# Kernel tuning notes

Hardware: AMD Instinct MI355X
Metric: run time of the kernel (lower is better)

The kernel has to match this reference:

```python
import jax, jax.numpy as jnp
import numpy as np

C = 512
NUM_HEADS = 8


def setup_inputs() -> dict:
    key = jax.random.key(0)
    ks = jax.random.split(key, 9)
    s = 1.0 / np.sqrt(C)
    inp = {
        "x": jax.random.normal(ks[0], (2, C, 64, 64), dtype=jnp.float32),
        "Wq": jax.random.uniform(ks[1], (C, C), jnp.float32, -s, s),
        "bq": jax.random.uniform(ks[2], (C,), jnp.float32, -s, s),
        "Wk": jax.random.uniform(ks[3], (C, C), jnp.float32, -s, s),
        "bk": jax.random.uniform(ks[4], (C,), jnp.float32, -s, s),
        "Wv": jax.random.uniform(ks[5], (C, C), jnp.float32, -s, s),
        "bv": jax.random.uniform(ks[6], (C,), jnp.float32, -s, s),
        "Wp": jax.random.uniform(ks[7], (C, C), jnp.float32, -s, s),
        "bp": jax.random.uniform(ks[8], (C,), jnp.float32, -s, s),
    }
    return inp


def _split_heads(t):
    # [B, S, C] -> [B, h, S, d]
    B, S, Ct = t.shape
    return t.reshape(B, S, NUM_HEADS, Ct // NUM_HEADS).transpose(0, 2, 1, 3)


def reference(x, Wq, bq, Wk, bk, Wv, bv, Wp, bp):
    B, Ct, H, W = x.shape
    tok = x.transpose(0, 2, 3, 1).reshape(B, H * W, Ct)  # [B, S, C]
    q = _split_heads(tok @ Wq.T + bq)
    k = _split_heads(tok @ Wk.T + bk)
    v = _split_heads(tok @ Wv.T + bv)
    d = q.shape[-1]
    scores = jnp.einsum("bhsd,bhtd->bhst", q, k) / jnp.sqrt(jnp.float32(d))
    attn = jax.nn.softmax(scores, axis=-1)
    out = jnp.einsum("bhst,bhtd->bhsd", attn, v)
    out = out.transpose(0, 2, 1, 3).reshape(B, H * W, Ct)  # merge heads
    out = out @ Wp.T + bp
    return out.reshape(B, H, W, Ct).transpose(0, 3, 1, 2)
```

## Files before the change

kernel.cpp:

```cpp
#include <hip/hip_runtime.h>
#include <stdint.h>
#include <math.h>

typedef unsigned short u16;
typedef uint32_t u32;
typedef short bf16x8 __attribute__((ext_vector_type(8)));
typedef float f32x4  __attribute__((ext_vector_type(4)));

#define DEV __device__ __forceinline__

DEV u16 f2bf(float f) {
    union { float f; u32 u; } x; x.f = f;
    u32 lsb = (x.u >> 16) & 1u;
    x.u += 0x7fffu + lsb;
    return (u16)(x.u >> 16);
}

DEV u32 pack2(float a, float b) {
    union { float f; u32 u; } x, y; x.f = a; y.f = b;
    return __builtin_amdgcn_perm(y.u + 0x8000u, x.u + 0x8000u, 0x07060302u);
}

#if __has_builtin(__builtin_amdgcn_exp2f)
DEV float fexp2(float x) { return __builtin_amdgcn_exp2f(x); }
#else
DEV float fexp2(float x) { return __expf(x * 0.69314718056f); }
#endif

DEV f32x4 mfma16(bf16x8 a, bf16x8 b, f32x4 c) {
    return __builtin_amdgcn_mfma_f32_16x16x32_bf16(a, b, c, 0, 0, 0);
}

__global__ __launch_bounds__(256) void prep_kernel(const float* __restrict__ x,
                                                   u16* __restrict__ tok,
                                                   const float* __restrict__ w0,
                                                   const float* __restrict__ w1,
                                                   const float* __restrict__ w2,
                                                   const float* __restrict__ w3,
                                                   u16* __restrict__ dst) {
    __shared__ u16 t[64][65];
    const int id = blockIdx.x, tid = threadIdx.x;
    if (id < 1024) {
        const int b = id >> 9, c0 = ((id >> 6) & 7) * 64, s0 = (id & 63) * 64;
        const float* xb = x + ((size_t)b * 512 + c0) * 4096 + s0;
        u16* tb = tok + ((size_t)b * 4096 + s0) * 512 + c0;
        {
            const int jc = tid & 15, i0 = tid >> 4;
#pragma unroll
            for (int ii = 0; ii < 4; ii++) {
                int i = i0 * 4 + ii;
                float4 v = *(const float4*)&xb[(size_t)i * 4096 + jc * 4];
                t[i][jc * 4 + 0] = f2bf(v.x);
                t[i][jc * 4 + 1] = f2bf(v.y);
                t[i][jc * 4 + 2] = f2bf(v.z);
                t[i][jc * 4 + 3] = f2bf(v.w);
            }
        }
        __syncthreads();
        {
            const int j = tid & 31, i0 = tid >> 5;
#pragma unroll
            for (int ii = 0; ii < 8; ii++) {
                int srow = i0 * 8 + ii;
                u32 v = (u32)t[j * 2][srow] | ((u32)t[j * 2 + 1][srow] << 16);
                *(u32*)(&tb[(size_t)srow * 512 + j * 2]) = v;
            }
        }
    } else {
        const int id2 = id - 1024;
        const int j = id2 >> 8;
        const float* src = (j == 0) ? w0 : (j == 1) ? w1 : (j == 2) ? w2 : w3;
        int idx = ((id2 & 255) * 256 + tid) * 4;
        float4 v = *(const float4*)&src[idx];
        uint2 pv;
        pv.x = pack2(v.x, v.y);
        pv.y = pack2(v.z, v.w);
        *(uint2*)&dst[(size_t)j * 262144 + idx] = pv;
    }
}

DEV void proj_core(const u16* __restrict__ W, const float* __restrict__ bias,
                   const u16* __restrict__ Bb, void* __restrict__ out,
                   int b, int mode, float scale,
                   u16 (*__restrict__ Alds)[4096], u16 (*__restrict__ Blds)[4096]) {
    const int tid = threadIdx.x;
    const int wave = tid >> 6, lane = tid & 63, q = lane >> 4, c = lane & 15;
    const int m0 = blockIdx.y * 128, n0 = blockIdx.x * 128;

    const int cs = tid & 15, qs = (tid >> 4) & 3, ms = (tid >> 6) & 3;
    const u16* Asrc0 = W  + (size_t)(m0 + ms * 16 + cs) * 512 + qs * 8;
    const u16* Asrc1 = W  + (size_t)(m0 + (ms + 4) * 16 + cs) * 512 + qs * 8;
    const u16* Bsrc0 = Bb + (size_t)(n0 + ms * 16 + cs) * 512 + qs * 8;
    const u16* Bsrc1 = Bb + (size_t)(n0 + (ms + 4) * 16 + cs) * 512 + qs * 8;

    f32x4 acc[4][4] = {};

    int4 pa0 = *(const int4*)&Asrc0[0];
    int4 pa1 = *(const int4*)&Asrc1[0];
    int4 pb0 = *(const int4*)&Bsrc0[0];
    int4 pb1 = *(const int4*)&Bsrc1[0];
    int4 ha0 = *(const int4*)&Asrc0[32];
    int4 ha1 = *(const int4*)&Asrc1[32];
    int4 hb0 = *(const int4*)&Bsrc0[32];
    int4 hb1 = *(const int4*)&Bsrc1[32];
    *(int4*)&Alds[0][tid * 8]         = pa0;
    *(int4*)&Alds[0][(tid + 256) * 8] = pa1;
    *(int4*)&Blds[0][tid * 8]         = pb0;
    *(int4*)&Blds[0][(tid + 256) * 8] = pb1;
    __syncthreads();

    int p = 0, pw = 1;
    for (int it = 0; it < 16; it++) {
        const int kn = ((it + 2) & 15) * 32;

        int4 na0 = *(const int4*)&Asrc0[kn];
        int4 na1 = *(const int4*)&Asrc1[kn];
        int4 nb0 = *(const int4*)&Bsrc0[kn];
        int4 nb1 = *(const int4*)&Bsrc1[kn];

        bf16x8 af[4], bfr[4];
#pragma unroll
        for (int t = 0; t < 4; t++) {
            int gm = (((wave & 1) * 4 + t) * 4 + q) * 16 + c;
            af[t] = *(const bf16x8*)&Alds[p][gm * 8];
            int gn = (((wave >> 1) * 4 + t) * 4 + q) * 16 + c;
            bfr[t] = *(const bf16x8*)&Blds[p][gn * 8];
        }
#pragma unroll
        for (int mt = 0; mt < 4; mt++)
#pragma unroll
            for (int nt = 0; nt < 4; nt++)
                acc[mt][nt] = mfma16(af[mt], bfr[nt], acc[mt][nt]);

        *(int4*)&Alds[pw][tid * 8]         = ha0;
        *(int4*)&Alds[pw][(tid + 256) * 8] = ha1;
        *(int4*)&Blds[pw][tid * 8]         = hb0;
        *(int4*)&Blds[pw][(tid + 256) * 8] = hb1;
        ha0 = na0; ha1 = na1; hb0 = nb0; hb1 = nb1;
        __syncthreads();
        p = pw; pw = (pw == 2) ? 0 : pw + 1;
    }

    const int mbase = m0 + (wave & 1) * 64, nbase = n0 + (wave >> 1) * 64;
#pragma unroll
    for (int mt = 0; mt < 4; mt++) {
        int co0 = mbase + mt * 16 + q * 4;
        float b0 = bias[co0 + 0], b1 = bias[co0 + 1];
        float b2 = bias[co0 + 2], b3 = bias[co0 + 3];
#pragma unroll
        for (int nt = 0; nt < 4; nt++) {
            int scol = nbase + nt * 16 + c;
            float v0 = (acc[mt][nt][0] + b0) * scale;
            float v1 = (acc[mt][nt][1] + b1) * scale;
            float v2 = (acc[mt][nt][2] + b2) * scale;
            float v3 = (acc[mt][nt][3] + b3) * scale;
            if (mode == 0) {
                uint2 pv; pv.x = pack2(v0, v1); pv.y = pack2(v2, v3);
                size_t idx = ((size_t)(b * 8 + (co0 >> 6)) * 4096 + scol) * 64 + (co0 & 63);
                *(uint2*)&((u16*)out)[idx] = pv;
            } else if (mode == 1) {
                u16* o = (u16*)out;
                o[((size_t)(b * 512 + co0 + 0)) * 4096 + scol] = f2bf(v0);
                o[((size_t)(b * 512 + co0 + 1)) * 4096 + scol] = f2bf(v1);
                o[((size_t)(b * 512 + co0 + 2)) * 4096 + scol] = f2bf(v2);
                o[((size_t)(b * 512 + co0 + 3)) * 4096 + scol] = f2bf(v3);
            } else {
                float* o = (float*)out;
                o[((size_t)(b * 512 + co0 + 0)) * 4096 + scol] = v0;
                o[((size_t)(b * 512 + co0 + 1)) * 4096 + scol] = v1;
                o[((size_t)(b * 512 + co0 + 2)) * 4096 + scol] = v2;
                o[((size_t)(b * 512 + co0 + 3)) * 4096 + scol] = v3;
            }
        }
    }
}

__global__ __launch_bounds__(256) void qkv_kernel(const u16* __restrict__ Wbf,
                                                  const float* __restrict__ bq,
                                                  const float* __restrict__ bk,
                                                  const float* __restrict__ bv,
                                                  const u16* __restrict__ tok,
                                                  u16* __restrict__ Qb,
                                                  u16* __restrict__ Kb,
                                                  u16* __restrict__ Vb) {
    __shared__ u16 Alds[3][4096];
    __shared__ u16 Blds[3][4096];
    const int z = blockIdx.z, j = z >> 1, b = z & 1;
    const u16* W = Wbf + (size_t)j * 262144;
    const float* bias = (j == 0) ? bq : (j == 1) ? bk : bv;
    void* out = (j == 0) ? (void*)Qb : (j == 1) ? (void*)Kb : (void*)Vb;
    const float scale = (j == 0) ? 0.1803368801f : 1.0f;
    const int mode = (j == 2) ? 1 : 0;
    proj_core(W, bias, tok + (size_t)b * (4096 * 512), out, b, mode, scale, Alds, Blds);
}

__global__ __launch_bounds__(256) void projp_kernel(const u16* __restrict__ Wp,
                                                    const float* __restrict__ bp,
                                                    const u16* __restrict__ attout,
                                                    float* __restrict__ out) {
    __shared__ u16 Alds[3][4096];
    __shared__ u16 Blds[3][4096];
    const int b = blockIdx.z;
    proj_core(Wp, bp, attout + (size_t)b * (4096 * 512), out, b, 2, 1.0f, Alds, Blds);
}

__global__ __launch_bounds__(256) void attn_kernel(const u16* __restrict__ Qm,
                                                   const u16* __restrict__ Km,
                                                   const u16* __restrict__ Vm,
                                                   u16* __restrict__ attout) {
    __shared__ u16 Klds[2][4096];
    __shared__ u16 Vlds[2][4096];
    __shared__ u16 Plds[128 * 72];
    const int tid = threadIdx.x, wave = tid >> 6, lane = tid & 63;
    const int q = lane >> 4, c = lane & 15;
    const int bhd = blockIdx.y, s0 = blockIdx.x * 128;
    const u16* Qb = Qm + (size_t)bhd * (4096 * 64);
    const u16* Kb = Km + (size_t)bhd * (4096 * 64);
    const u16* Vb = Vm + (size_t)bhd * (64 * 4096);

    bf16x8 qf[2][2];
#pragma unroll
    for (int st = 0; st < 2; st++)
#pragma unroll
        for (int kd = 0; kd < 2; kd++)
            qf[st][kd] = *(const bf16x8*)
                &Qb[(size_t)(s0 + wave * 32 + st * 16 + c) * 64 + kd * 32 + q * 8];

    const int rr = tid & 15, qq = (tid >> 4) & 3, kk = (tid >> 6) & 1;
    const int t40 = tid >> 7, t41 = t40 + 2;
    const u16* Ksrc0 = Kb + (size_t)(t40 * 16 + rr) * 64 + kk * 32 + qq * 8;
    const u16* Ksrc1 = Kb + (size_t)(t41 * 16 + rr) * 64 + kk * 32 + qq * 8;
    const u16* Vsrc0 = Vb + (size_t)(t40 * 16 + rr) * 4096 + kk * 32 + qq * 8;
    const u16* Vsrc1 = Vb + (size_t)(t41 * 16 + rr) * 4096 + kk * 32 + qq * 8;
    u16* Prow = &Plds[(size_t)(wave * 32 + c) * 72];

    f32x4 oacc[4][2] = {};
    float lsum[2] = {0.f, 0.f};

    *(int4*)&Klds[0][tid * 8]         = *(const int4*)&Ksrc0[0];
    *(int4*)&Klds[0][(tid + 256) * 8] = *(const int4*)&Ksrc1[0];
    *(int4*)&Vlds[0][tid * 8]         = *(const int4*)&Vsrc0[0];
    *(int4*)&Vlds[0][(tid + 256) * 8] = *(const int4*)&Vsrc1[0];
    __syncthreads();

    for (int it = 0; it < 64; it++) {
        const int p = it & 1;
        const size_t t0n = (size_t)(((it + 1) & 63) * 64);

        int4 kst0 = *(const int4*)&Ksrc0[t0n * 64];
        int4 kst1 = *(const int4*)&Ksrc1[t0n * 64];
        int4 vst0 = *(const int4*)&Vsrc0[t0n];
        int4 vst1 = *(const int4*)&Vsrc1[t0n];

        f32x4 sacc[4][2] = {};
#pragma unroll
        for (int kd = 0; kd < 2; kd++) {
            bf16x8 ka[4];
#pragma unroll
            for (int tt = 0; tt < 4; tt++)
                ka[tt] = *(const bf16x8*)&Klds[p][(((tt * 2 + kd) * 4 + q) * 16 + c) * 8];
#pragma unroll
            for (int tt = 0; tt < 4; tt++)
#pragma unroll
                for (int st = 0; st < 2; st++)
                    sacc[tt][st] = mfma16(ka[tt], qf[st][kd], sacc[tt][st]);
        }

#pragma unroll
        for (int st = 0; st < 2; st++) {
#pragma unroll
            for (int tt = 0; tt < 4; tt++) {
                float p0 = fexp2(sacc[tt][st][0]);
                float p1 = fexp2(sacc[tt][st][1]);
                float p2 = fexp2(sacc[tt][st][2]);
                float p3 = fexp2(sacc[tt][st][3]);
                lsum[st] += (p0 + p1) + (p2 + p3);
                uint2 pv; pv.x = pack2(p0, p1); pv.y = pack2(p2, p3);
                *(uint2*)&Prow[st * (16 * 72) + tt * 16 + q * 4] = pv;
            }
        }

#pragma unroll
        for (int kt = 0; kt < 2; kt++) {
            bf16x8 va[4], pb[2];
#pragma unroll
            for (int dt = 0; dt < 4; dt++)
                va[dt] = *(const bf16x8*)&Vlds[p][(((dt * 2 + kt) * 4 + q) * 16 + c) * 8];
#pragma unroll
            for (int st = 0; st < 2; st++)
                pb[st] = *(const bf16x8*)&Prow[st * (16 * 72) + kt * 32 + q * 8];
#pragma unroll
            for (int dt = 0; dt < 4; dt++)
#pragma unroll
                for (int st = 0; st < 2; st++)
                    oacc[dt][st] = mfma16(va[dt], pb[st], oacc[dt][st]);
        }

        *(int4*)&Klds[1 - p][tid * 8]         = kst0;
        *(int4*)&Klds[1 - p][(tid + 256) * 8] = kst1;
        *(int4*)&Vlds[1 - p][tid * 8]         = vst0;
        *(int4*)&Vlds[1 - p][(tid + 256) * 8] = vst1;
        __syncthreads();
    }

    const int b = bhd >> 3, hd = bhd & 7;
#pragma unroll
    for (int st = 0; st < 2; st++) {
        float l = lsum[st];
        l += __shfl_xor(l, 16, 64);
        l += __shfl_xor(l, 32, 64);
        float rl = 1.0f / l;
        int s = s0 + wave * 32 + st * 16 + c;
#pragma unroll
        for (int dt = 0; dt < 4; dt++) {
            uint2 pv;
            pv.x = pack2(oacc[dt][st][0] * rl, oacc[dt][st][1] * rl);
            pv.y = pack2(oacc[dt][st][2] * rl, oacc[dt][st][3] * rl);
            size_t idx = ((size_t)(b * 4096 + s)) * 512 + hd * 64 + dt * 16 + q * 4;
            *(uint2*)&attout[idx] = pv;
        }
    }
}

extern "C" void kernel_launch(void* const* d_in, const int* in_sizes, int n_in,
                              void* d_out, int out_size, void* d_ws, size_t ws_size,
                              hipStream_t stream) {
    (void)in_sizes; (void)n_in; (void)out_size; (void)ws_size;
    const float* x  = (const float*)d_in[0];
    const float* Wq = (const float*)d_in[1];
    const float* bq = (const float*)d_in[2];
    const float* Wk = (const float*)d_in[3];
    const float* bk = (const float*)d_in[4];
    const float* Wv = (const float*)d_in[5];
    const float* bv = (const float*)d_in[6];
    const float* Wp = (const float*)d_in[7];
    const float* bp = (const float*)d_in[8];
    float* out = (float*)d_out;

    const size_t NTOK = (size_t)4 * 1024 * 1024;
    u16* tok = (u16*)d_ws;
    u16* Qb  = tok + NTOK;
    u16* Kb  = Qb + NTOK;
    u16* Vb  = Kb + NTOK;
    u16* Wbf = Vb + NTOK;
    u16* attout = tok;

    prep_kernel<<<dim3(2048), 256, 0, stream>>>(x, tok, Wq, Wk, Wv, Wp, Wbf);
    qkv_kernel<<<dim3(32, 4, 6), 256, 0, stream>>>(Wbf, bq, bk, bv, tok, Qb, Kb, Vb);
    attn_kernel<<<dim3(32, 16), 256, 0, stream>>>(Qb, Kb, Vb, attout);
    projp_kernel<<<dim3(32, 4, 2), 256, 0, stream>>>(Wbf + 3 * 262144, bp, attout, out);
}
```

Measured before the change: 224.4 us.

## Fuse all stages into one persistent cooperative kernel with grid syncs

Replaces the four separate launches (prep, QKV projection, attention, output projection) with a single 512-block cooperative kernel. Grid-wide syncs separate the phases, and a static job assignment gives 256 blocks a second QKV tile. The stages share one LDS buffer, and a fallback launches the same kernel four times with a phase argument if the cooperative launch fails. The goal is to remove inter-kernel launch gaps and tail drain. The risks are grid-sync overhead, uneven work in the QKV phase, and register and occupancy limits set by the heaviest phase.

```diff
diff --git a/kernel.cpp b/kernel.cpp
--- a/kernel.cpp
+++ b/kernel.cpp
@@ -1,6 +1,9 @@
 #include <hip/hip_runtime.h>
+#include <hip/hip_cooperative_groups.h>
 #include <stdint.h>
 #include <math.h>
+
+namespace cg = cooperative_groups;
 
 typedef unsigned short u16;
 typedef uint32_t u32;
@@ -31,61 +34,55 @@
     return __builtin_amdgcn_mfma_f32_16x16x32_bf16(a, b, c, 0, 0, 0);
 }
 
-__global__ __launch_bounds__(256) void prep_kernel(const float* __restrict__ x,
-                                                   u16* __restrict__ tok,
-                                                   const float* __restrict__ w0,
-                                                   const float* __restrict__ w1,
-                                                   const float* __restrict__ w2,
-                                                   const float* __restrict__ w3,
-                                                   u16* __restrict__ dst) {
-    __shared__ u16 t[64][65];
-    const int id = blockIdx.x, tid = threadIdx.x;
-    if (id < 1024) {
-        const int b = id >> 9, c0 = ((id >> 6) & 7) * 64, s0 = (id & 63) * 64;
-        const float* xb = x + ((size_t)b * 512 + c0) * 4096 + s0;
-        u16* tb = tok + ((size_t)b * 4096 + s0) * 512 + c0;
-        {
-            const int jc = tid & 15, i0 = tid >> 4;
-#pragma unroll
-            for (int ii = 0; ii < 4; ii++) {
-                int i = i0 * 4 + ii;
-                float4 v = *(const float4*)&xb[(size_t)i * 4096 + jc * 4];
-                t[i][jc * 4 + 0] = f2bf(v.x);
-                t[i][jc * 4 + 1] = f2bf(v.y);
-                t[i][jc * 4 + 2] = f2bf(v.z);
-                t[i][jc * 4 + 3] = f2bf(v.w);
-            }
-        }
-        __syncthreads();
-        {
-            const int j = tid & 31, i0 = tid >> 5;
-#pragma unroll
-            for (int ii = 0; ii < 8; ii++) {
-                int srow = i0 * 8 + ii;
-                u32 v = (u32)t[j * 2][srow] | ((u32)t[j * 2 + 1][srow] << 16);
-                *(u32*)(&tb[(size_t)srow * 512 + j * 2]) = v;
-            }
-        }
-    } else {
-        const int id2 = id - 1024;
-        const int j = id2 >> 8;
-        const float* src = (j == 0) ? w0 : (j == 1) ? w1 : (j == 2) ? w2 : w3;
-        int idx = ((id2 & 255) * 256 + tid) * 4;
-        float4 v = *(const float4*)&src[idx];
-        uint2 pv;
-        pv.x = pack2(v.x, v.y);
-        pv.y = pack2(v.z, v.w);
-        *(uint2*)&dst[(size_t)j * 262144 + idx] = pv;
-    }
-}
-
-DEV void proj_core(const u16* __restrict__ W, const float* __restrict__ bias,
+DEV void do_transpose(int id, const float* __restrict__ x, u16* __restrict__ tok,
+                      u16* __restrict__ t) {
+    const int tid = threadIdx.x;
+    const int b = id >> 9, c0 = ((id >> 6) & 7) * 64, s0 = (id & 63) * 64;
+    const float* xb = x + ((size_t)b * 512 + c0) * 4096 + s0;
+    u16* tb = tok + ((size_t)b * 4096 + s0) * 512 + c0;
+    {
+        const int jc = tid & 15, i0 = tid >> 4;
+#pragma unroll
+        for (int ii = 0; ii < 4; ii++) {
+            int i = i0 * 4 + ii;
+            float4 v = *(const float4*)&xb[(size_t)i * 4096 + jc * 4];
+            t[i * 65 + jc * 4 + 0] = f2bf(v.x);
+            t[i * 65 + jc * 4 + 1] = f2bf(v.y);
+            t[i * 65 + jc * 4 + 2] = f2bf(v.z);
+            t[i * 65 + jc * 4 + 3] = f2bf(v.w);
+        }
+    }
+    __syncthreads();
+    {
+        const int j = tid & 31, i0 = tid >> 5;
+#pragma unroll
+        for (int ii = 0; ii < 8; ii++) {
+            int srow = i0 * 8 + ii;
+            u32 v = (u32)t[(j * 2) * 65 + srow] | ((u32)t[(j * 2 + 1) * 65 + srow] << 16);
+            *(u32*)(&tb[(size_t)srow * 512 + j * 2]) = v;
+        }
+    }
+}
+
+DEV void do_wconv(int id, const float* __restrict__ w0, const float* __restrict__ w1,
+                  const float* __restrict__ w2, const float* __restrict__ w3,
+                  u16* __restrict__ dst) {
+    const int j = id >> 8;
+    const float* src = (j == 0) ? w0 : (j == 1) ? w1 : (j == 2) ? w2 : w3;
+    int idx = ((id & 255) * 256 + threadIdx.x) * 4;
+    float4 v = *(const float4*)&src[idx];
+    uint2 pv;
+    pv.x = pack2(v.x, v.y);
+    pv.y = pack2(v.z, v.w);
+    *(uint2*)&dst[(size_t)j * 262144 + idx] = pv;
+}
+
+DEV void proj_tile(const u16* __restrict__ W, const float* __restrict__ bias,
                    const u16* __restrict__ Bb, void* __restrict__ out,
-                   int b, int mode, float scale,
-                   u16 (*__restrict__ Alds)[4096], u16 (*__restrict__ Blds)[4096]) {
+                   int b, int mode, float scale, int m0, int n0,
+                   u16* __restrict__ Ab, u16* __restrict__ Bl) {
     const int tid = threadIdx.x;
     const int wave = tid >> 6, lane = tid & 63, q = lane >> 4, c = lane & 15;
-    const int m0 = blockIdx.y * 128, n0 = blockIdx.x * 128;
 
     const int cs = tid & 15, qs = (tid >> 4) & 3, ms = (tid >> 6) & 3;
     const u16* Asrc0 = W  + (size_t)(m0 + ms * 16 + cs) * 512 + qs * 8;
@@ -103,10 +100,10 @@
     int4 ha1 = *(const int4*)&Asrc1[32];
     int4 hb0 = *(const int4*)&Bsrc0[32];
     int4 hb1 = *(const int4*)&Bsrc1[32];
-    *(int4*)&Alds[0][tid * 8]         = pa0;
-    *(int4*)&Alds[0][(tid + 256) * 8] = pa1;
-    *(int4*)&Blds[0][tid * 8]         = pb0;
-    *(int4*)&Blds[0][(tid + 256) * 8] = pb1;
+    *(int4*)&Ab[tid * 8]         = pa0;
+    *(int4*)&Ab[(tid + 256) * 8] = pa1;
+    *(int4*)&Bl[tid * 8]         = pb0;
+    *(int4*)&Bl[(tid + 256) * 8] = pb1;
     __syncthreads();
 
     int p = 0, pw = 1;
@@ -122,9 +119,9 @@
 #pragma unroll
         for (int t = 0; t < 4; t++) {
             int gm = (((wave & 1) * 4 + t) * 4 + q) * 16 + c;
-            af[t] = *(const bf16x8*)&Alds[p][gm * 8];
+            af[t] = *(const bf16x8*)&Ab[p * 4096 + gm * 8];
             int gn = (((wave >> 1) * 4 + t) * 4 + q) * 16 + c;
-            bfr[t] = *(const bf16x8*)&Blds[p][gn * 8];
+            bfr[t] = *(const bf16x8*)&Bl[p * 4096 + gn * 8];
         }
 #pragma unroll
         for (int mt = 0; mt < 4; mt++)
@@ -132,10 +129,10 @@
             for (int nt = 0; nt < 4; nt++)
                 acc[mt][nt] = mfma16(af[mt], bfr[nt], acc[mt][nt]);
 
-        *(int4*)&Alds[pw][tid * 8]         = ha0;
-        *(int4*)&Alds[pw][(tid + 256) * 8] = ha1;
-        *(int4*)&Blds[pw][tid * 8]         = hb0;
-        *(int4*)&Blds[pw][(tid + 256) * 8] = hb1;
+        *(int4*)&Ab[pw * 4096 + tid * 8]         = ha0;
+        *(int4*)&Ab[pw * 4096 + (tid + 256) * 8] = ha1;
+        *(int4*)&Bl[pw * 4096 + tid * 8]         = hb0;
+        *(int4*)&Bl[pw * 4096 + (tid + 256) * 8] = hb1;
         ha0 = na0; ha1 = na1; hb0 = nb0; hb1 = nb1;
         __syncthreads();
         p = pw; pw = (pw == 2) ? 0 : pw + 1;
@@ -175,45 +172,12 @@
     }
 }
 
-__global__ __launch_bounds__(256) void qkv_kernel(const u16* __restrict__ Wbf,
-                                                  const float* __restrict__ bq,
-                                                  const float* __restrict__ bk,
-                                                  const float* __restrict__ bv,
-                                                  const u16* __restrict__ tok,
-                                                  u16* __restrict__ Qb,
-                                                  u16* __restrict__ Kb,
-                                                  u16* __restrict__ Vb) {
-    __shared__ u16 Alds[3][4096];
-    __shared__ u16 Blds[3][4096];
-    const int z = blockIdx.z, j = z >> 1, b = z & 1;
-    const u16* W = Wbf + (size_t)j * 262144;
-    const float* bias = (j == 0) ? bq : (j == 1) ? bk : bv;
-    void* out = (j == 0) ? (void*)Qb : (j == 1) ? (void*)Kb : (void*)Vb;
-    const float scale = (j == 0) ? 0.1803368801f : 1.0f;
-    const int mode = (j == 2) ? 1 : 0;
-    proj_core(W, bias, tok + (size_t)b * (4096 * 512), out, b, mode, scale, Alds, Blds);
-}
-
-__global__ __launch_bounds__(256) void projp_kernel(const u16* __restrict__ Wp,
-                                                    const float* __restrict__ bp,
-                                                    const u16* __restrict__ attout,
-                                                    float* __restrict__ out) {
-    __shared__ u16 Alds[3][4096];
-    __shared__ u16 Blds[3][4096];
-    const int b = blockIdx.z;
-    proj_core(Wp, bp, attout + (size_t)b * (4096 * 512), out, b, 2, 1.0f, Alds, Blds);
-}
-
-__global__ __launch_bounds__(256) void attn_kernel(const u16* __restrict__ Qm,
-                                                   const u16* __restrict__ Km,
-                                                   const u16* __restrict__ Vm,
-                                                   u16* __restrict__ attout) {
-    __shared__ u16 Klds[2][4096];
-    __shared__ u16 Vlds[2][4096];
-    __shared__ u16 Plds[128 * 72];
+DEV void attn_tile(int s0, int bhd,
+                   const u16* __restrict__ Qm, const u16* __restrict__ Km,
+                   const u16* __restrict__ Vm, u16* __restrict__ attout,
+                   u16* __restrict__ Kl, u16* __restrict__ Vl, u16* __restrict__ Pl) {
     const int tid = threadIdx.x, wave = tid >> 6, lane = tid & 63;
     const int q = lane >> 4, c = lane & 15;
-    const int bhd = blockIdx.y, s0 = blockIdx.x * 128;
     const u16* Qb = Qm + (size_t)bhd * (4096 * 64);
     const u16* Kb = Km + (size_t)bhd * (4096 * 64);
     const u16* Vb = Vm + (size_t)bhd * (64 * 4096);
@@ -232,15 +196,15 @@
     const u16* Ksrc1 = Kb + (size_t)(t41 * 16 + rr) * 64 + kk * 32 + qq * 8;
     const u16* Vsrc0 = Vb + (size_t)(t40 * 16 + rr) * 4096 + kk * 32 + qq * 8;
     const u16* Vsrc1 = Vb + (size_t)(t41 * 16 + rr) * 4096 + kk * 32 + qq * 8;
-    u16* Prow = &Plds[(size_t)(wave * 32 + c) * 72];
+    u16* Prow = &Pl[(size_t)(wave * 32 + c) * 72];
 
     f32x4 oacc[4][2] = {};
     float lsum[2] = {0.f, 0.f};
 
-    *(int4*)&Klds[0][tid * 8]         = *(const int4*)&Ksrc0[0];
-    *(int4*)&Klds[0][(tid + 256) * 8] = *(const int4*)&Ksrc1[0];
-    *(int4*)&Vlds[0][tid * 8]         = *(const int4*)&Vsrc0[0];
-    *(int4*)&Vlds[0][(tid + 256) * 8] = *(const int4*)&Vsrc1[0];
+    *(int4*)&Kl[tid * 8]         = *(const int4*)&Ksrc0[0];
+    *(int4*)&Kl[(tid + 256) * 8] = *(const int4*)&Ksrc1[0];
+    *(int4*)&Vl[tid * 8]         = *(const int4*)&Vsrc0[0];
+    *(int4*)&Vl[(tid + 256) * 8] = *(const int4*)&Vsrc1[0];
     __syncthreads();
 
     for (int it = 0; it < 64; it++) {
@@ -258,7 +222,7 @@
             bf16x8 ka[4];
 #pragma unroll
             for (int tt = 0; tt < 4; tt++)
-                ka[tt] = *(const bf16x8*)&Klds[p][(((tt * 2 + kd) * 4 + q) * 16 + c) * 8];
+                ka[tt] = *(const bf16x8*)&Kl[p * 4096 + (((tt * 2 + kd) * 4 + q) * 16 + c) * 8];
 #pragma unroll
             for (int tt = 0; tt < 4; tt++)
 #pragma unroll
@@ -285,7 +249,7 @@
             bf16x8 va[4], pb[2];
 #pragma unroll
             for (int dt = 0; dt < 4; dt++)
-                va[dt] = *(const bf16x8*)&Vlds[p][(((dt * 2 + kt) * 4 + q) * 16 + c) * 8];
+                va[dt] = *(const bf16x8*)&Vl[p * 4096 + (((dt * 2 + kt) * 4 + q) * 16 + c) * 8];
 #pragma unroll
             for (int st = 0; st < 2; st++)
                 pb[st] = *(const bf16x8*)&Prow[st * (16 * 72) + kt * 32 + q * 8];
@@ -296,10 +260,10 @@
                     oacc[dt][st] = mfma16(va[dt], pb[st], oacc[dt][st]);
         }
 
-        *(int4*)&Klds[1 - p][tid * 8]         = kst0;
-        *(int4*)&Klds[1 - p][(tid + 256) * 8] = kst1;
-        *(int4*)&Vlds[1 - p][tid * 8]         = vst0;
-        *(int4*)&Vlds[1 - p][(tid + 256) * 8] = vst1;
+        *(int4*)&Kl[(1 - p) * 4096 + tid * 8]         = kst0;
+        *(int4*)&Kl[(1 - p) * 4096 + (tid + 256) * 8] = kst1;
+        *(int4*)&Vl[(1 - p) * 4096 + tid * 8]         = vst0;
+        *(int4*)&Vl[(1 - p) * 4096 + (tid + 256) * 8] = vst1;
         __syncthreads();
     }
 
@@ -319,6 +283,61 @@
             size_t idx = ((size_t)(b * 4096 + s)) * 512 + hd * 64 + dt * 16 + q * 4;
             *(uint2*)&attout[idx] = pv;
         }
+    }
+}
+
+__global__ __launch_bounds__(256) void fused_kernel(
+    int phase, int coop,
+    const float* __restrict__ x,
+    const float* __restrict__ Wq, const float* __restrict__ bq,
+    const float* __restrict__ Wk, const float* __restrict__ bk,
+    const float* __restrict__ Wv, const float* __restrict__ bv,
+    const float* __restrict__ Wp, const float* __restrict__ bp,
+    u16* __restrict__ tok, u16* __restrict__ Qb, u16* __restrict__ Kb,
+    u16* __restrict__ Vb, u16* __restrict__ Wbf, u16* __restrict__ attout,
+    float* __restrict__ out) {
+    __shared__ __align__(16) u16 sm[25600];
+    const int wg = blockIdx.x;
+
+    if (phase <= 0) {
+        do_transpose(wg, x, tok, sm);
+        __syncthreads();
+        do_transpose(wg + 512, x, tok, sm);
+        do_wconv(wg, Wq, Wk, Wv, Wp, Wbf);
+        do_wconv(wg + 512, Wq, Wk, Wv, Wp, Wbf);
+    }
+    if (coop) cg::this_grid().sync();
+
+    if (phase == -1 || phase == 1) {
+        int job = wg;
+        for (;;) {
+            int pb = job >> 7, t = job & 127;
+            int j = pb >> 1, b = pb & 1;
+            int m0 = (t >> 5) * 128, n0 = (t & 31) * 128;
+            const u16* W = Wbf + (size_t)j * 262144;
+            const float* bias = (j == 0) ? bq : (j == 1) ? bk : bv;
+            void* o = (j == 0) ? (void*)Qb : (j == 1) ? (void*)Kb : (void*)Vb;
+            float scale = (j == 0) ? 0.1803368801f : 1.0f;
+            int mode = (j == 2) ? 1 : 0;
+            proj_tile(W, bias, tok + (size_t)b * (4096 * 512), o, b, mode, scale,
+                      m0, n0, sm, sm + 12288);
+            if (phase == -1 && wg < 256 && job == wg) { job = wg + 512; continue; }
+            break;
+        }
+    }
+    if (coop) cg::this_grid().sync();
+
+    if (phase == -1 || phase == 2) {
+        attn_tile((wg & 31) * 128, wg >> 5, Qb, Kb, Vb, attout,
+                  sm, sm + 8192, sm + 16384);
+    }
+    if (coop) cg::this_grid().sync();
+
+    if ((phase == -1 && wg < 256) || phase == 3) {
+        int b = wg >> 7, t = wg & 127;
+        int m0 = (t >> 5) * 128, n0 = (t & 31) * 128;
+        proj_tile(Wbf + (size_t)3 * 262144, bp, attout + (size_t)b * (4096 * 512),
+                  out, b, 2, 1.0f, m0, n0, sm, sm + 12288);
     }
 }
 
@@ -345,8 +364,20 @@
     u16* Wbf = Vb + NTOK;
     u16* attout = tok;
 
-    prep_kernel<<<dim3(2048), 256, 0, stream>>>(x, tok, Wq, Wk, Wv, Wp, Wbf);
-    qkv_kernel<<<dim3(32, 4, 6), 256, 0, stream>>>(Wbf, bq, bk, bv, tok, Qb, Kb, Vb);
-    attn_kernel<<<dim3(32, 16), 256, 0, stream>>>(Qb, Kb, Vb, attout);
-    projp_kernel<<<dim3(32, 4, 2), 256, 0, stream>>>(Wbf + 3 * 262144, bp, attout, out);
-}
+    int phase = -1, coop = 1;
+    void* args[] = {&phase, &coop, &x, &Wq, &bq, &Wk, &bk, &Wv, &bv, &Wp, &bp,
+                    &tok, &Qb, &Kb, &Vb, &Wbf, &attout, &out};
+    hipError_t e = hipLaunchCooperativeKernel((const void*)fused_kernel,
+                                              dim3(512), dim3(256), args, 0, stream);
+    if (e != hipSuccess) {
+        (void)hipGetLastError();
+        fused_kernel<<<512, 256, 0, stream>>>(0, 0, x, Wq, bq, Wk, bk, Wv, bv, Wp, bp,
+                                              tok, Qb, Kb, Vb, Wbf, attout, out);
+        fused_kernel<<<768, 256, 0, stream>>>(1, 0, x, Wq, bq, Wk, bk, Wv, bv, Wp, bp,
+                                              tok, Qb, Kb, Vb, Wbf, attout, out);
+        fused_kernel<<<512, 256, 0, stream>>>(2, 0, x, Wq, bq, Wk, bk, Wv, bv, Wp, bp,
+                                              tok, Qb, Kb, Vb, Wbf, attout, out);
+        fused_kernel<<<256, 256, 0, stream>>>(3, 0, x, Wq, bq, Wk, bk, Wv, bv, Wp, bp,
+                                              tok, Qb, Kb, Vb, Wbf, attout, out);
+    }
+}
```

Measured after the change: 426.2 us. +89.9%, slower.

## Fuse fp32 weight conversion into projection GEMMs and halve output-projection M tile

Applied to the files above, without the earlier changes.

The separate weight-to-bf16 pass in the prep kernel is removed. The QKV and output-projection GEMMs now load fp32 weights directly and pack them to bf16 while staging into LDS. The output projection also gets its own kernel with 64-row M tiles, doubling its block count to improve occupancy across CUs. The cost is re-reading fp32 weights (twice the bytes) from every block and doing conversion arithmetic inside the GEMM loop.

```diff
diff --git a/kernel.cpp b/kernel.cpp
--- a/kernel.cpp
+++ b/kernel.cpp
@@ -21,6 +21,13 @@
     return __builtin_amdgcn_perm(y.u + 0x8000u, x.u + 0x8000u, 0x07060302u);
 }
 
+DEV int4 packA(float4 lo, float4 hi) {
+    int4 r;
+    r.x = pack2(lo.x, lo.y); r.y = pack2(lo.z, lo.w);
+    r.z = pack2(hi.x, hi.y); r.w = pack2(hi.z, hi.w);
+    return r;
+}
+
 #if __has_builtin(__builtin_amdgcn_exp2f)
 DEV float fexp2(float x) { return __builtin_amdgcn_exp2f(x); }
 #else
@@ -32,89 +39,73 @@
 }
 
 __global__ __launch_bounds__(256) void prep_kernel(const float* __restrict__ x,
-                                                   u16* __restrict__ tok,
-                                                   const float* __restrict__ w0,
-                                                   const float* __restrict__ w1,
-                                                   const float* __restrict__ w2,
-                                                   const float* __restrict__ w3,
-                                                   u16* __restrict__ dst) {
+                                                   u16* __restrict__ tok) {
     __shared__ u16 t[64][65];
     const int id = blockIdx.x, tid = threadIdx.x;
-    if (id < 1024) {
-        const int b = id >> 9, c0 = ((id >> 6) & 7) * 64, s0 = (id & 63) * 64;
-        const float* xb = x + ((size_t)b * 512 + c0) * 4096 + s0;
-        u16* tb = tok + ((size_t)b * 4096 + s0) * 512 + c0;
-        {
-            const int jc = tid & 15, i0 = tid >> 4;
-#pragma unroll
-            for (int ii = 0; ii < 4; ii++) {
-                int i = i0 * 4 + ii;
-                float4 v = *(const float4*)&xb[(size_t)i * 4096 + jc * 4];
-                t[i][jc * 4 + 0] = f2bf(v.x);
-                t[i][jc * 4 + 1] = f2bf(v.y);
-                t[i][jc * 4 + 2] = f2bf(v.z);
-                t[i][jc * 4 + 3] = f2bf(v.w);
-            }
-        }
-        __syncthreads();
-        {
-            const int j = tid & 31, i0 = tid >> 5;
-#pragma unroll
-            for (int ii = 0; ii < 8; ii++) {
-                int srow = i0 * 8 + ii;
-                u32 v = (u32)t[j * 2][srow] | ((u32)t[j * 2 + 1][srow] << 16);
-                *(u32*)(&tb[(size_t)srow * 512 + j * 2]) = v;
-            }
-        }
-    } else {
-        const int id2 = id - 1024;
-        const int j = id2 >> 8;
-        const float* src = (j == 0) ? w0 : (j == 1) ? w1 : (j == 2) ? w2 : w3;
-        int idx = ((id2 & 255) * 256 + tid) * 4;
-        float4 v = *(const float4*)&src[idx];
-        uint2 pv;
-        pv.x = pack2(v.x, v.y);
-        pv.y = pack2(v.z, v.w);
-        *(uint2*)&dst[(size_t)j * 262144 + idx] = pv;
-    }
-}
-
-DEV void proj_core(const u16* __restrict__ W, const float* __restrict__ bias,
-                   const u16* __restrict__ Bb, void* __restrict__ out,
-                   int b, int mode, float scale,
-                   u16 (*__restrict__ Alds)[4096], u16 (*__restrict__ Blds)[4096]) {
+    const int b = id >> 9, c0 = ((id >> 6) & 7) * 64, s0 = (id & 63) * 64;
+    const float* xb = x + ((size_t)b * 512 + c0) * 4096 + s0;
+    u16* tb = tok + ((size_t)b * 4096 + s0) * 512 + c0;
+    {
+        const int jc = tid & 15, i0 = tid >> 4;
+#pragma unroll
+        for (int ii = 0; ii < 4; ii++) {
+            int i = i0 * 4 + ii;
+            float4 v = *(const float4*)&xb[(size_t)i * 4096 + jc * 4];
+            t[i][jc * 4 + 0] = f2bf(v.x);
+            t[i][jc * 4 + 1] = f2bf(v.y);
+            t[i][jc * 4 + 2] = f2bf(v.z);
+            t[i][jc * 4 + 3] = f2bf(v.w);
+        }
+    }
+    __syncthreads();
+    {
+        const int j = tid & 31, i0 = tid >> 5;
+#pragma unroll
+        for (int ii = 0; ii < 8; ii++) {
+            int srow = i0 * 8 + ii;
+            u32 v = (u32)t[j * 2][srow] | ((u32)t[j * 2 + 1][srow] << 16);
+            *(u32*)(&tb[(size_t)srow * 512 + j * 2]) = v;
+        }
+    }
+}
+
+DEV void proj128(const float* __restrict__ W, const float* __restrict__ bias,
+                 const u16* __restrict__ Bb, void* __restrict__ out,
+                 int b, int mode, float scale, int m0, int n0,
+                 u16* __restrict__ Ab, u16* __restrict__ Bl) {
     const int tid = threadIdx.x;
     const int wave = tid >> 6, lane = tid & 63, q = lane >> 4, c = lane & 15;
-    const int m0 = blockIdx.y * 128, n0 = blockIdx.x * 128;
 
     const int cs = tid & 15, qs = (tid >> 4) & 3, ms = (tid >> 6) & 3;
-    const u16* Asrc0 = W  + (size_t)(m0 + ms * 16 + cs) * 512 + qs * 8;
-    const u16* Asrc1 = W  + (size_t)(m0 + (ms + 4) * 16 + cs) * 512 + qs * 8;
+    const float* Asrc0 = W + (size_t)(m0 + ms * 16 + cs) * 512 + qs * 8;
+    const float* Asrc1 = W + (size_t)(m0 + (ms + 4) * 16 + cs) * 512 + qs * 8;
     const u16* Bsrc0 = Bb + (size_t)(n0 + ms * 16 + cs) * 512 + qs * 8;
     const u16* Bsrc1 = Bb + (size_t)(n0 + (ms + 4) * 16 + cs) * 512 + qs * 8;
 
     f32x4 acc[4][4] = {};
 
-    int4 pa0 = *(const int4*)&Asrc0[0];
-    int4 pa1 = *(const int4*)&Asrc1[0];
-    int4 pb0 = *(const int4*)&Bsrc0[0];
-    int4 pb1 = *(const int4*)&Bsrc1[0];
-    int4 ha0 = *(const int4*)&Asrc0[32];
-    int4 ha1 = *(const int4*)&Asrc1[32];
+    {
+        float4 a0lo = *(const float4*)&Asrc0[0], a0hi = *(const float4*)&Asrc0[4];
+        float4 a1lo = *(const float4*)&Asrc1[0], a1hi = *(const float4*)&Asrc1[4];
+        int4 b0 = *(const int4*)&Bsrc0[0];
+        int4 b1 = *(const int4*)&Bsrc1[0];
+        *(int4*)&Ab[tid * 8]         = packA(a0lo, a0hi);
+        *(int4*)&Ab[(tid + 256) * 8] = packA(a1lo, a1hi);
+        *(int4*)&Bl[tid * 8]         = b0;
+        *(int4*)&Bl[(tid + 256) * 8] = b1;
+    }
+    float4 h0lo = *(const float4*)&Asrc0[32], h0hi = *(const float4*)&Asrc0[36];
+    float4 h1lo = *(const float4*)&Asrc1[32], h1hi = *(const float4*)&Asrc1[36];
     int4 hb0 = *(const int4*)&Bsrc0[32];
     int4 hb1 = *(const int4*)&Bsrc1[32];
-    *(int4*)&Alds[0][tid * 8]         = pa0;
-    *(int4*)&Alds[0][(tid + 256) * 8] = pa1;
-    *(int4*)&Blds[0][tid * 8]         = pb0;
-    *(int4*)&Blds[0][(tid + 256) * 8] = pb1;
     __syncthreads();
 
     int p = 0, pw = 1;
     for (int it = 0; it < 16; it++) {
         const int kn = ((it + 2) & 15) * 32;
 
-        int4 na0 = *(const int4*)&Asrc0[kn];
-        int4 na1 = *(const int4*)&Asrc1[kn];
+        float4 na0lo = *(const float4*)&Asrc0[kn], na0hi = *(const float4*)&Asrc0[kn + 4];
+        float4 na1lo = *(const float4*)&Asrc1[kn], na1hi = *(const float4*)&Asrc1[kn + 4];
         int4 nb0 = *(const int4*)&Bsrc0[kn];
         int4 nb1 = *(const int4*)&Bsrc1[kn];
 
@@ -122,9 +113,9 @@
 #pragma unroll
         for (int t = 0; t < 4; t++) {
             int gm = (((wave & 1) * 4 + t) * 4 + q) * 16 + c;
-            af[t] = *(const bf16x8*)&Alds[p][gm * 8];
+            af[t] = *(const bf16x8*)&Ab[p * 4096 + gm * 8];
             int gn = (((wave >> 1) * 4 + t) * 4 + q) * 16 + c;
-            bfr[t] = *(const bf16x8*)&Blds[p][gn * 8];
+            bfr[t] = *(const bf16x8*)&Bl[p * 4096 + gn * 8];
         }
 #pragma unroll
         for (int mt = 0; mt < 4; mt++)
@@ -132,11 +123,12 @@
             for (int nt = 0; nt < 4; nt++)
                 acc[mt][nt] = mfma16(af[mt], bfr[nt], acc[mt][nt]);
 
-        *(int4*)&Alds[pw][tid * 8]         = ha0;
-        *(int4*)&Alds[pw][(tid + 256) * 8] = ha1;
-        *(int4*)&Blds[pw][tid * 8]         = hb0;
-        *(int4*)&Blds[pw][(tid + 256) * 8] = hb1;
-        ha0 = na0; ha1 = na1; hb0 = nb0; hb1 = nb1;
+        *(int4*)&Ab[pw * 4096 + tid * 8]         = packA(h0lo, h0hi);
+        *(int4*)&Ab[pw * 4096 + (tid + 256) * 8] = packA(h1lo, h1hi);
+        *(int4*)&Bl[pw * 4096 + tid * 8]         = hb0;
+        *(int4*)&Bl[pw * 4096 + (tid + 256) * 8] = hb1;
+        h0lo = na0lo; h0hi = na0hi; h1lo = na1lo; h1hi = na1hi;
+        hb0 = nb0; hb1 = nb1;
         __syncthreads();
         p = pw; pw = (pw == 2) ? 0 : pw + 1;
     }
@@ -158,50 +150,109 @@
                 uint2 pv; pv.x = pack2(v0, v1); pv.y = pack2(v2, v3);
                 size_t idx = ((size_t)(b * 8 + (co0 >> 6)) * 4096 + scol) * 64 + (co0 & 63);
                 *(uint2*)&((u16*)out)[idx] = pv;
-            } else if (mode == 1) {
+            } else {
                 u16* o = (u16*)out;
                 o[((size_t)(b * 512 + co0 + 0)) * 4096 + scol] = f2bf(v0);
                 o[((size_t)(b * 512 + co0 + 1)) * 4096 + scol] = f2bf(v1);
                 o[((size_t)(b * 512 + co0 + 2)) * 4096 + scol] = f2bf(v2);
                 o[((size_t)(b * 512 + co0 + 3)) * 4096 + scol] = f2bf(v3);
-            } else {
-                float* o = (float*)out;
-                o[((size_t)(b * 512 + co0 + 0)) * 4096 + scol] = v0;
-                o[((size_t)(b * 512 + co0 + 1)) * 4096 + scol] = v1;
-                o[((size_t)(b * 512 + co0 + 2)) * 4096 + scol] = v2;
-                o[((size_t)(b * 512 + co0 + 3)) * 4096 + scol] = v3;
             }
         }
     }
 }
 
-__global__ __launch_bounds__(256) void qkv_kernel(const u16* __restrict__ Wbf,
-                                                  const float* __restrict__ bq,
-                                                  const float* __restrict__ bk,
-                                                  const float* __restrict__ bv,
-                                                  const u16* __restrict__ tok,
-                                                  u16* __restrict__ Qb,
-                                                  u16* __restrict__ Kb,
-                                                  u16* __restrict__ Vb) {
-    __shared__ u16 Alds[3][4096];
-    __shared__ u16 Blds[3][4096];
+__global__ __launch_bounds__(256) void qkv_kernel(
+    const float* __restrict__ Wq, const float* __restrict__ bq,
+    const float* __restrict__ Wk, const float* __restrict__ bk,
+    const float* __restrict__ Wv, const float* __restrict__ bv,
+    const u16* __restrict__ tok,
+    u16* __restrict__ Qb, u16* __restrict__ Kb, u16* __restrict__ Vb) {
+    __shared__ __align__(16) u16 Alds[3 * 4096];
+    __shared__ __align__(16) u16 Blds[3 * 4096];
     const int z = blockIdx.z, j = z >> 1, b = z & 1;
-    const u16* W = Wbf + (size_t)j * 262144;
+    const float* W = (j == 0) ? Wq : (j == 1) ? Wk : Wv;
     const float* bias = (j == 0) ? bq : (j == 1) ? bk : bv;
     void* out = (j == 0) ? (void*)Qb : (j == 1) ? (void*)Kb : (void*)Vb;
     const float scale = (j == 0) ? 0.1803368801f : 1.0f;
     const int mode = (j == 2) ? 1 : 0;
-    proj_core(W, bias, tok + (size_t)b * (4096 * 512), out, b, mode, scale, Alds, Blds);
-}
-
-__global__ __launch_bounds__(256) void projp_kernel(const u16* __restrict__ Wp,
+    proj128(W, bias, tok + (size_t)b * (4096 * 512), out, b, mode, scale,
+            blockIdx.y * 128, blockIdx.x * 128, Alds, Blds);
+}
+
+__global__ __launch_bounds__(256) void projp_kernel(const float* __restrict__ Wp,
                                                     const float* __restrict__ bp,
-                                                    const u16* __restrict__ attout,
+                                                    const u16* __restrict__ attin,
                                                     float* __restrict__ out) {
-    __shared__ u16 Alds[3][4096];
-    __shared__ u16 Blds[3][4096];
-    const int b = blockIdx.z;
-    proj_core(Wp, bp, attout + (size_t)b * (4096 * 512), out, b, 2, 1.0f, Alds, Blds);
+    __shared__ __align__(16) u16 Ab[3 * 2048];
+    __shared__ __align__(16) u16 Bl[3 * 4096];
+    const int tid = threadIdx.x;
+    const int wave = tid >> 6, lane = tid & 63, q = lane >> 4, c = lane & 15;
+    const int m0 = blockIdx.y * 64, n0 = blockIdx.x * 128, b = blockIdx.z;
+    const u16* Bb = attin + (size_t)b * (4096 * 512);
+
+    const int cs = tid & 15, qs = (tid >> 4) & 3, ms = (tid >> 6) & 3;
+    const float* Asrc = Wp + (size_t)(m0 + ms * 16 + cs) * 512 + qs * 8;
+    const u16* Bsrc0 = Bb + (size_t)(n0 + ms * 16 + cs) * 512 + qs * 8;
+    const u16* Bsrc1 = Bb + (size_t)(n0 + (ms + 4) * 16 + cs) * 512 + qs * 8;
+
+    f32x4 acc[4][2] = {};
+
+    {
+        float4 alo = *(const float4*)&Asrc[0], ahi = *(const float4*)&Asrc[4];
+        int4 b0 = *(const int4*)&Bsrc0[0];
+        int4 b1 = *(const int4*)&Bsrc1[0];
+        *(int4*)&Ab[tid * 8] = packA(alo, ahi);
+        *(int4*)&Bl[tid * 8]         = b0;
+        *(int4*)&Bl[(tid + 256) * 8] = b1;
+    }
+    float4 hlo = *(const float4*)&Asrc[32], hhi = *(const float4*)&Asrc[36];
+    int4 hb0 = *(const int4*)&Bsrc0[32];
+    int4 hb1 = *(const int4*)&Bsrc1[32];
+    __syncthreads();
+
+    int p = 0, pw = 1;
+    for (int it = 0; it < 16; it++) {
+        const int kn = ((it + 2) & 15) * 32;
+
+        float4 nlo = *(const float4*)&Asrc[kn], nhi = *(const float4*)&Asrc[kn + 4];
+        int4 nb0 = *(const int4*)&Bsrc0[kn];
+        int4 nb1 = *(const int4*)&Bsrc1[kn];
+
+        bf16x8 af[4], bfr[2];
+#pragma unroll
+        for (int mt = 0; mt < 4; mt++)
+            af[mt] = *(const bf16x8*)&Ab[p * 2048 + ((mt * 4 + q) * 16 + c) * 8];
+#pragma unroll
+        for (int nt = 0; nt < 2; nt++)
+            bfr[nt] = *(const bf16x8*)&Bl[p * 4096 + (((wave * 2 + nt) * 4 + q) * 16 + c) * 8];
+#pragma unroll
+        for (int mt = 0; mt < 4; mt++)
+#pragma unroll
+            for (int nt = 0; nt < 2; nt++)
+                acc[mt][nt] = mfma16(af[mt], bfr[nt], acc[mt][nt]);
+
+        *(int4*)&Ab[pw * 2048 + tid * 8] = packA(hlo, hhi);
+        *(int4*)&Bl[pw * 4096 + tid * 8]         = hb0;
+        *(int4*)&Bl[pw * 4096 + (tid + 256) * 8] = hb1;
+        hlo = nlo; hhi = nhi; hb0 = nb0; hb1 = nb1;
+        __syncthreads();
+        p = pw; pw = (pw == 2) ? 0 : pw + 1;
+    }
+
+#pragma unroll
+    for (int mt = 0; mt < 4; mt++) {
+        int co0 = m0 + mt * 16 + q * 4;
+        float b0 = bp[co0 + 0], b1 = bp[co0 + 1];
+        float b2 = bp[co0 + 2], b3 = bp[co0 + 3];
+#pragma unroll
+        for (int nt = 0; nt < 2; nt++) {
+            int scol = n0 + wave * 32 + nt * 16 + c;
+            out[((size_t)(b * 512 + co0 + 0)) * 4096 + scol] = acc[mt][nt][0] + b0;
+            out[((size_t)(b * 512 + co0 + 1)) * 4096 + scol] = acc[mt][nt][1] + b1;
+            out[((size_t)(b * 512 + co0 + 2)) * 4096 + scol] = acc[mt][nt][2] + b2;
+            out[((size_t)(b * 512 + co0 + 3)) * 4096 + scol] = acc[mt][nt][3] + b3;
+        }
+    }
 }
 
 __global__ __launch_bounds__(256) void attn_kernel(const u16* __restrict__ Qm,
@@ -342,11 +393,10 @@
     u16* Qb  = tok + NTOK;
     u16* Kb  = Qb + NTOK;
     u16* Vb  = Kb + NTOK;
-    u16* Wbf = Vb + NTOK;
     u16* attout = tok;
 
-    prep_kernel<<<dim3(2048), 256, 0, stream>>>(x, tok, Wq, Wk, Wv, Wp, Wbf);
-    qkv_kernel<<<dim3(32, 4, 6), 256, 0, stream>>>(Wbf, bq, bk, bv, tok, Qb, Kb, Vb);
+    prep_kernel<<<dim3(1024), 256, 0, stream>>>(x, tok);
+    qkv_kernel<<<dim3(32, 4, 6), 256, 0, stream>>>(Wq, bq, Wk, bk, Wv, bv, tok, Qb, Kb, Vb);
     attn_kernel<<<dim3(32, 16), 256, 0, stream>>>(Qb, Kb, Vb, attout);
-    projp_kernel<<<dim3(32, 4, 2), 256, 0, stream>>>(Wbf + 3 * 262144, bp, attout, out);
-}
+    projp_kernel<<<dim3(32, 8, 2), 256, 0, stream>>>(Wp, bp, attout, out);
+}
```

After: 249.1 us. 1.11x slower.
